# Kernel optimization log

Hardware: AMD Instinct MI355X
Metric: run time of the kernel (lower is better)

Reference implementation:

```python
import jax, jax.numpy as jnp
import numpy as np

D_MODEL = 2048
NHEAD = 32
GROUPS = 8
HEAD_DIM = D_MODEL // NHEAD  # 64
HPG = NHEAD // GROUPS        # heads per group = 4
ROPE_BASE = 10000.0


def _rope(x):
    # x: [B, H, S, D] -- rotate-half RoPE over full head dim, matching RoPE module
    S, D = x.shape[2], x.shape[3]
    theta = 1.0 / (ROPE_BASE ** (jnp.arange(0, D, 2, dtype=jnp.float32) / D))  # [D/2]
    idx_theta = jnp.arange(S, dtype=jnp.float32)[:, None] * theta[None, :]     # [S, D/2]
    ang = jnp.concatenate([idx_theta, idx_theta], axis=-1)                     # [S, D]
    cos = jnp.cos(ang)[None, None]  # [1,1,S,D]
    sin = jnp.sin(ang)[None, None]
    d2 = D // 2
    neg_half = jnp.concatenate([-x[..., d2:], x[..., :d2]], axis=-1)
    return x * cos + neg_half * sin


def setup_inputs() -> dict:
    key = jax.random.key(0)
    ks = jax.random.split(key, 9)
    B, S = 2, 2048
    s_in = 1.0 / np.sqrt(D_MODEL)
    return {
        "x": jax.random.normal(ks[0], (B, S, D_MODEL), jnp.float32),
        "Wq": jax.random.normal(ks[1], (D_MODEL, D_MODEL), jnp.float32) * s_in,
        "bq": jax.random.normal(ks[2], (D_MODEL,), jnp.float32) * 0.01,
        "Wk": jax.random.normal(ks[3], (HEAD_DIM * GROUPS, D_MODEL), jnp.float32) * s_in,
        "bk": jax.random.normal(ks[4], (HEAD_DIM * GROUPS,), jnp.float32) * 0.01,
        "Wv": jax.random.normal(ks[5], (HEAD_DIM * GROUPS, D_MODEL), jnp.float32) * s_in,
        "bv": jax.random.normal(ks[6], (HEAD_DIM * GROUPS,), jnp.float32) * 0.01,
        "Wo": jax.random.normal(ks[7], (D_MODEL, D_MODEL), jnp.float32) * s_in,
        "bo": jax.random.normal(ks[8], (D_MODEL,), jnp.float32) * 0.01,
    }


def reference(x, Wq, bq, Wk, bk, Wv, bv, Wo, bo):
    B, S, _ = x.shape
    # projections (torch Linear: x @ W.T + b)
    q = (x @ Wq.T + bq).reshape(B, S, NHEAD, HEAD_DIM).transpose(0, 2, 1, 3)   # [B,H,S,D]
    k = (x @ Wk.T + bk).reshape(B, S, GROUPS, HEAD_DIM).transpose(0, 2, 1, 3)  # [B,G,S,D]
    v = (x @ Wv.T + bv).reshape(B, S, GROUPS, HEAD_DIM).transpose(0, 2, 1, 3)  # [B,G,S,D]
    q = _rope(q)
    k = _rope(k)
    # grouped-query attention: share each k/v group across HPG query heads
    qg = q.reshape(B, GROUPS, HPG, S, HEAD_DIM)
    scale = 1.0 / np.sqrt(HEAD_DIM)
    scores = jnp.einsum('bghsd,bgtd->bghst', qg, k) * scale  # [B,G,Hpg,S,S]
    causal = jnp.tril(jnp.ones((S, S), dtype=bool))
    scores = jnp.where(causal, scores, jnp.finfo(scores.dtype).min)
    attn = jax.nn.softmax(scores, axis=-1)
    out = jnp.einsum('bghst,bgtd->bghsd', attn, v)           # [B,G,Hpg,S,D]
    out = out.reshape(B, NHEAD, S, HEAD_DIM).transpose(0, 2, 1, 3).reshape(B, S, D_MODEL)
    return out @ Wo.T + bo
```

## Files before the change

kernel.cpp:

```cpp
#include <hip/hip_runtime.h>

typedef unsigned short u16;
typedef __bf16 bf16x8 __attribute__((ext_vector_type(8)));
typedef float floatx4 __attribute__((ext_vector_type(4)));
typedef u16 u16x8 __attribute__((ext_vector_type(8)));
typedef u16 u16x4 __attribute__((ext_vector_type(4)));

#define D_MODEL 2048
#define S_LEN   2048
#define BATCH   2
#define NHEAD   32
#define GROUPS  8
#define HEAD_DIM 64
#define KV_DIM  512

__device__ __forceinline__ float bf2f(u16 h) {
  unsigned int u = ((unsigned int)h) << 16;
  return __builtin_bit_cast(float, u);
}
__device__ __forceinline__ u16 f2bf(float f) {
  unsigned int u = __builtin_bit_cast(unsigned int, f);
  u += 0x7fffu + ((u >> 16) & 1u);
  return (u16)(u >> 16);
}
__device__ __forceinline__ float fexp2(float x) {
  float r;
  asm("v_exp_f32 %0, %1" : "=v"(r) : "v"(x));
  return r;
}

#define GLD_LDS(gp, lp) \
  __builtin_amdgcn_global_load_lds((__attribute__((address_space(1))) void*)(gp), \
                                   (__attribute__((address_space(3))) void*)(lp), 16, 0, 0)

__global__ __launch_bounds__(256)
void cvt5_f32_bf16(const float* s0, const float* s1, const float* s2,
                   const float* s3, const float* s4,
                   u16* d0, u16* d1, u16* d2, u16* d3, u16* d4,
                   int n0, int n1, int n2, int n3, int n4,
                   float* ct, float* st)
{
  if (blockIdx.y == 5) {
    int idx = blockIdx.x * 256 + threadIdx.x;
    if (idx < S_LEN * 32) {
      int s = idx >> 5, d = idx & 31;
      float theta = __expf(-(float)d * 0.28782313662425574f);
      float sn, cs;
      sincosf((float)s * theta, &sn, &cs);
      ct[idx] = cs; st[idx] = sn;
    }
    return;
  }
  const float* s; u16* d; int n;
  switch (blockIdx.y) {
    case 0: s = s0; d = d0; n = n0; break;
    case 1: s = s1; d = d1; n = n1; break;
    case 2: s = s2; d = d2; n = n2; break;
    case 3: s = s3; d = d3; n = n3; break;
    default: s = s4; d = d4; n = n4; break;
  }
  long i = ((long)blockIdx.x * 256 + threadIdx.x) * 8;
  if (i >= n) return;
  floatx4 a = *(const floatx4*)(s + i);
  floatx4 b = *(const floatx4*)(s + i + 4);
  u16x8 r;
#pragma unroll
  for (int j = 0; j < 4; ++j) { r[j] = f2bf(a[j]); r[4 + j] = f2bf(b[j]); }
  *(u16x8*)(d + i) = r;
}

__global__ __launch_bounds__(256, 3)
void gemm_qkv(const u16* __restrict__ A, const u16* __restrict__ Wq,
              const u16* __restrict__ Wkv,
              const float* __restrict__ bq, const float* __restrict__ bk,
              const float* __restrict__ bv,
              u16* __restrict__ Qb, u16* __restrict__ Kb, u16* __restrict__ Vt,
              const float* __restrict__ ct, const float* __restrict__ st)
{
  const int K = D_MODEL;
  __shared__ __align__(16) u16 As[2 * 128 * 32];
  __shared__ __align__(16) u16 Bs[2 * 128 * 32];
  const int t = threadIdx.x;
  const int w = t >> 6, l = t & 63;
  const int lr = l & 15, lq = l >> 4;
  const int wm = (w >> 1) * 64, wn = (w & 1) * 64;
  const long bm = (long)blockIdx.x * 128;

  const bool isQ = blockIdx.y < 16;
  const long bn = isQ ? (long)blockIdx.y * 128 : (long)(blockIdx.y - 16) * 128;
  const u16* W = isQ ? Wq : Wkv;

  floatx4 acc[4][4] = {};

  const u16* a0 = A + (bm + (t >> 2)) * (long)K + (t & 3) * 8;
  const u16* a1 = a0 + 64L * K;
  const u16* pB0 = W + (bn + (t >> 2)) * (long)K + (t & 3) * 8;
  const u16* pB1 = pB0 + 64L * K;
  u16* As0 = As + w * 512;
  u16* As1 = As + 2048 + w * 512;
  u16* Bs0 = Bs + w * 512;
  u16* Bs1 = Bs + 2048 + w * 512;

  for (int k0 = 0; k0 < K; k0 += 64) {
    GLD_LDS(a0 + k0, As0);
    GLD_LDS(a1 + k0, As1);
    GLD_LDS(pB0 + k0, Bs0);
    GLD_LDS(pB1 + k0, Bs1);
    GLD_LDS(a0 + k0 + 32, As0 + 4096);
    GLD_LDS(a1 + k0 + 32, As1 + 4096);
    GLD_LDS(pB0 + k0 + 32, Bs0 + 4096);
    GLD_LDS(pB1 + k0 + 32, Bs1 + 4096);
    __syncthreads();

#pragma unroll
    for (int kk = 0; kk < 2; ++kk) {
      const u16* as = As + kk * 4096;
      const u16* bs = Bs + kk * 4096;
      bf16x8 av[4], bv8[4];
#pragma unroll
      for (int i = 0; i < 4; ++i)
        av[i] = *(const bf16x8*)(as + (wm + i * 16 + lr) * 32 + lq * 8);
#pragma unroll
      for (int j = 0; j < 4; ++j)
        bv8[j] = *(const bf16x8*)(bs + (wn + j * 16 + lr) * 32 + lq * 8);
#pragma unroll
      for (int i = 0; i < 4; ++i)
#pragma unroll
        for (int j = 0; j < 4; ++j)
          acc[i][j] = __builtin_amdgcn_mfma_f32_16x16x32_bf16(av[i], bv8[j], acc[i][j], 0, 0, 0);
    }
    __syncthreads();
  }

  if (isQ || bn < KV_DIM) {
    const float* bias = isQ ? bq : bk;
    u16* dst = isQ ? Qb : Kb;
    const long ldc = isQ ? D_MODEL : KV_DIM;
    float bb[4];
#pragma unroll
    for (int j = 0; j < 4; ++j)
      bb[j] = bias[bn + wn + j * 16 + lr];
#pragma unroll
    for (int i = 0; i < 4; ++i) {
#pragma unroll
      for (int rr = 0; rr < 4; ++rr) {
        long row = bm + wm + i * 16 + lq * 4 + rr;
        int srow = (int)row & (S_LEN - 1);
        float c0 = ct[srow * 32 + lr],      sn0 = st[srow * 32 + lr];
        float c1 = ct[srow * 32 + 16 + lr], sn1 = st[srow * 32 + 16 + lr];
        float v0 = acc[i][0][rr] + bb[0];
        float v1 = acc[i][1][rr] + bb[1];
        float v2 = acc[i][2][rr] + bb[2];
        float v3 = acc[i][3][rr] + bb[3];
        u16* cp = dst + row * ldc + bn + wn + lr;
        cp[0]  = f2bf(v0 * c0 - v2 * sn0);
        cp[16] = f2bf(v1 * c1 - v3 * sn1);
        cp[32] = f2bf(v2 * c0 + v0 * sn0);
        cp[48] = f2bf(v3 * c1 + v1 * sn1);
      }
    }
  } else {
    float bb[4];
#pragma unroll
    for (int j = 0; j < 4; ++j)
      bb[j] = bv[bn - KV_DIM + wn + j * 16 + lr];
#pragma unroll
    for (int i = 0; i < 4; ++i) {
      int row0 = (int)bm + wm + i * 16 + lq * 4;
      int b = row0 >> 11, s0r = row0 & (S_LEN - 1);
#pragma unroll
      for (int j = 0; j < 4; ++j) {
        int vcol = (int)bn - KV_DIM + wn + j * 16 + lr;
        u16x4 pv;
#pragma unroll
        for (int rr = 0; rr < 4; ++rr)
          pv[rr] = f2bf(acc[i][j][rr] + bb[j]);
        *(u16x4*)(Vt + ((long)b * KV_DIM + vcol) * S_LEN + s0r) = pv;
      }
    }
  }
}

__global__ __launch_bounds__(256, 3)
void gemm_out(const u16* __restrict__ A, const u16* __restrict__ W,
              const float* __restrict__ bias, float* __restrict__ C,
              int K, int ldc)
{
  __shared__ __align__(16) u16 As[2 * 128 * 32];
  __shared__ __align__(16) u16 Bs[2 * 128 * 32];
  const int t = threadIdx.x;
  const int w = t >> 6, l = t & 63;
  const int lr = l & 15, lq = l >> 4;
  const int wm = (w >> 1) * 64, wn = (w & 1) * 64;
  const long bm = (long)blockIdx.x * 128;
  const long bn = (long)blockIdx.y * 128;

  floatx4 acc[4][4] = {};

  const u16* a0 = A + (bm + (t >> 2)) * (long)K + (t & 3) * 8;
  const u16* a1 = a0 + 64L * K;
  const u16* pB0 = W + (bn + (t >> 2)) * (long)K + (t & 3) * 8;
  const u16* pB1 = pB0 + 64L * K;
  u16* As0 = As + w * 512;
  u16* As1 = As + 2048 + w * 512;
  u16* Bs0 = Bs + w * 512;
  u16* Bs1 = Bs + 2048 + w * 512;

  for (int k0 = 0; k0 < K; k0 += 64) {
    GLD_LDS(a0 + k0, As0);
    GLD_LDS(a1 + k0, As1);
    GLD_LDS(pB0 + k0, Bs0);
    GLD_LDS(pB1 + k0, Bs1);
    GLD_LDS(a0 + k0 + 32, As0 + 4096);
    GLD_LDS(a1 + k0 + 32, As1 + 4096);
    GLD_LDS(pB0 + k0 + 32, Bs0 + 4096);
    GLD_LDS(pB1 + k0 + 32, Bs1 + 4096);
    __syncthreads();

#pragma unroll
    for (int kk = 0; kk < 2; ++kk) {
      const u16* as = As + kk * 4096;
      const u16* bs = Bs + kk * 4096;
      bf16x8 av[4], bv[4];
#pragma unroll
      for (int i = 0; i < 4; ++i)
        av[i] = *(const bf16x8*)(as + (wm + i * 16 + lr) * 32 + lq * 8);
#pragma unroll
      for (int j = 0; j < 4; ++j)
        bv[j] = *(const bf16x8*)(bs + (wn + j * 16 + lr) * 32 + lq * 8);
#pragma unroll
      for (int i = 0; i < 4; ++i)
#pragma unroll
        for (int j = 0; j < 4; ++j)
          acc[i][j] = __builtin_amdgcn_mfma_f32_16x16x32_bf16(av[i], bv[j], acc[i][j], 0, 0, 0);
    }
    __syncthreads();
  }

  float bb[4];
#pragma unroll
  for (int j = 0; j < 4; ++j)
    bb[j] = bias[bn + wn + j * 16 + lr];
#pragma unroll
  for (int i = 0; i < 4; ++i) {
#pragma unroll
    for (int rr = 0; rr < 4; ++rr) {
      long row = bm + wm + i * 16 + lq * 4 + rr;
      long cidx = row * (long)ldc + bn + wn + lr;
      float* cp = C + cidx;
#pragma unroll
      for (int j = 0; j < 4; ++j)
        cp[j * 16] = acc[i][j][rr] + bb[j];
    }
  }
}

__global__ __launch_bounds__(256, 3)
void gqa_attn(const u16* Q, const u16* __restrict__ Kc,
              const u16* __restrict__ Vt, u16* O)
{
  __shared__ __align__(16) u16 KV[2][16 * 512];
  __shared__ __align__(16) u16 Ps[4][2][16 * 72];

  const int pr = blockIdx.x;
  const int bh = blockIdx.y;
  const int b = bh >> 5, h = bh & 31, g = h >> 2;

  const int t = threadIdx.x;
  const int w = t >> 6, l = t & 63;
  const int lr = l & 15, lq = l >> 4;

  const u16* Kp = Kc + ((long)b * S_LEN) * KV_DIM + g * HEAD_DIM;
  const u16* Vp = Vt + ((long)b * KV_DIM + g * HEAD_DIM) * S_LEN;

  long sb[4];
  {
    const int sig2 = ((l >> 2) ^ (l >> 4)) & 1;
    const int sig1 = ((l >> 1) ^ (l >> 3)) & 1;
    const int sig0 = (l ^ sig2) & 1;
    const int row = ((l >> 2) & 14) | sig2;
    const int cl = ((sig1 << 1) | sig0) * 8;
#pragma unroll
    for (int q = 0; q < 4; ++q) {
      const int r = (w & 1) * 4 + q;
      const int jj = r >> 1, cc = r & 1;
      sb[q] = (w < 2) ? ((long)(jj * 16 + row) * KV_DIM + cc * 32 + cl)
                      : ((long)(jj * 16 + row) * S_LEN + cc * 32 + cl);
    }
  }
  const u16* sp = (w < 2) ? Kp : Vp;
  const long smul = (w < 2) ? (long)64 * KV_DIM : 64;
  const int dbase = ((w < 2) ? 0 : 4096) + (w & 1) * 2048;
  const int koff = ((4 * lr + lq) ^ (lr & 7)) * 8;

  bf16x8 onesf;
#pragma unroll
  for (int e = 0; e < 8; ++e) onesf[e] = (__bf16)1.0f;

#define STAGE(bufi, kt_) do { \
    const long soff_ = (long)(kt_) * smul; \
    GLD_LDS(sp + soff_ + sb[0], &KV[bufi][dbase + 0 * 512]); \
    GLD_LDS(sp + soff_ + sb[1], &KV[bufi][dbase + 1 * 512]); \
    GLD_LDS(sp + soff_ + sb[2], &KV[bufi][dbase + 2 * 512]); \
    GLD_LDS(sp + soff_ + sb[3], &KV[bufi][dbase + 3 * 512]); \
  } while (0)

#define TILE(ktv, D0, D1) do { \
    const u16* buf_ = &KV[(ktv) & 1][0]; \
    floatx4 z0[4] = {}, z1[4] = {}; \
    _Pragma("unroll") \
    for (int j = 0; j < 4; ++j) { \
      bf16x8 kf0 = *(const bf16x8*)(buf_ + j * 1024 + koff); \
      bf16x8 kf1 = *(const bf16x8*)(buf_ + j * 1024 + 512 + koff); \
      if (!(D1) && (!(D0) || j <= w)) { \
        z0[j] = __builtin_amdgcn_mfma_f32_16x16x32_bf16(kf0, qf00, z0[j], 0, 0, 0); \
        z0[j] = __builtin_amdgcn_mfma_f32_16x16x32_bf16(kf1, qf01, z0[j], 0, 0, 0); \
      } \
      if (!(D1) || j <= w) { \
        z1[j] = __builtin_amdgcn_mfma_f32_16x16x32_bf16(kf0, qf10, z1[j], 0, 0, 0); \
        z1[j] = __builtin_amdgcn_mfma_f32_16x16x32_bf16(kf1, qf11, z1[j], 0, 0, 0); \
      } \
    } \
    if (!(D1)) { \
      _Pragma("unroll") \
      for (int j = 0; j < 4; ++j) { \
        u16x4 pk; \
        _Pragma("unroll") \
        for (int rr = 0; rr < 4; ++rr) { \
          float ps; \
          if ((D0) && (j * 16 + lq * 4 + rr > w * 16 + lr)) ps = 0.f; \
          else ps = fexp2(z0[j][rr] * 0.18033688011112042f - 23.083120654223414f); \
          pk[rr] = __builtin_bit_cast(u16, (__bf16)ps); \
        } \
        *(u16x4*)&Ps[w][0][lr * 72 + j * 16 + lq * 4] = pk; \
      } \
    } \
    _Pragma("unroll") \
    for (int j = 0; j < 4; ++j) { \
      u16x4 pk; \
      _Pragma("unroll") \
      for (int rr = 0; rr < 4; ++rr) { \
        float ps; \
        if ((D1) && (j * 16 + lq * 4 + rr > w * 16 + lr)) ps = 0.f; \
        else ps = fexp2(z1[j][rr] * 0.18033688011112042f - 23.083120654223414f); \
        pk[rr] = __builtin_bit_cast(u16, (__bf16)ps); \
      } \
      *(u16x4*)&Ps[w][1][lr * 72 + j * 16 + lq * 4] = pk; \
    } \
    bf16x8 pa00 = *(const bf16x8*)&Ps[w][0][lr * 72 + lq * 8]; \
    bf16x8 pa01 = *(const bf16x8*)&Ps[w][0][lr * 72 + 32 + lq * 8]; \
    bf16x8 pa10 = *(const bf16x8*)&Ps[w][1][lr * 72 + lq * 8]; \
    bf16x8 pa11 = *(const bf16x8*)&Ps[w][1][lr * 72 + 32 + lq * 8]; \
    if (!(D1)) { \
      lsa0 = __builtin_amdgcn_mfma_f32_16x16x32_bf16(pa00, onesf, lsa0, 0, 0, 0); \
      if (!(D0) || w >= 2) \
        lsa0 = __builtin_amdgcn_mfma_f32_16x16x32_bf16(pa01, onesf, lsa0, 0, 0, 0); \
    } \
    lsa1 = __builtin_amdgcn_mfma_f32_16x16x32_bf16(pa10, onesf, lsa1, 0, 0, 0); \
    if (!(D1) || w >= 2) \
      lsa1 = __builtin_amdgcn_mfma_f32_16x16x32_bf16(pa11, onesf, lsa1, 0, 0, 0); \
    const u16* vbuf_ = buf_ + 4096; \
    _Pragma("unroll") \
    for (int j = 0; j < 4; ++j) { \
      bf16x8 vb0 = *(const bf16x8*)(vbuf_ + j * 1024 + koff); \
      bf16x8 vb1 = *(const bf16x8*)(vbuf_ + j * 1024 + 512 + koff); \
      if (!(D1)) { \
        o0[j] = __builtin_amdgcn_mfma_f32_16x16x32_bf16(pa00, vb0, o0[j], 0, 0, 0); \
        if (!(D0) || w >= 2) \
          o0[j] = __builtin_amdgcn_mfma_f32_16x16x32_bf16(pa01, vb1, o0[j], 0, 0, 0); \
      } \
      o1[j] = __builtin_amdgcn_mfma_f32_16x16x32_bf16(pa10, vb0, o1[j], 0, 0, 0); \
      if (!(D1) || w >= 2) \
        o1[j] = __builtin_amdgcn_mfma_f32_16x16x32_bf16(pa11, vb1, o1[j], 0, 0, 0); \
    } \
  } while (0)

#pragma unroll 1
  for (int seg = 0; seg < 2; ++seg) {
    const int qt = seg ? (15 - pr) : pr;
    const u16* Qp = Q + ((long)b * S_LEN + qt * 128) * D_MODEL + h * HEAD_DIM;
    u16* Op = O + ((long)b * S_LEN + qt * 128) * D_MODEL + h * HEAD_DIM;

    bf16x8 qf00, qf01, qf10, qf11;
    {
      const u16* qr0 = Qp + (long)(w * 16 + lr) * D_MODEL;
      qf00 = *(const bf16x8*)(qr0 + lq * 8);
      qf01 = *(const bf16x8*)(qr0 + 32 + lq * 8);
      const u16* qr1 = qr0 + (long)64 * D_MODEL;
      qf10 = *(const bf16x8*)(qr1 + lq * 8);
      qf11 = *(const bf16x8*)(qr1 + 32 + lq * 8);
    }

    floatx4 o0[4] = {}, o1[4] = {};
    floatx4 lsa0 = {}, lsa1 = {};
    const int NKT = 2 * qt + 2;

    if (seg) __syncthreads();
    STAGE(0, 0);
    for (int kt = 0; kt < NKT - 2; ++kt) {
      __syncthreads();
      STAGE((kt + 1) & 1, kt + 1);
      TILE(kt, false, false);
    }
    __syncthreads();
    STAGE((NKT - 1) & 1, NKT - 1);
    TILE(NKT - 2, true, false);
    __syncthreads();
    TILE(NKT - 1, false, true);

#pragma unroll
    for (int s = 0; s < 2; ++s) {
      const floatx4 lsv = s ? lsa1 : lsa0;
      const floatx4* oo = s ? o1 : o0;
#pragma unroll
      for (int rr = 0; rr < 4; ++rr) {
        float inv = 1.f / lsv[rr];
        long row = s * 64 + w * 16 + lq * 4 + rr;
        u16* op = Op + row * (long)D_MODEL + lr;
#pragma unroll
        for (int j = 0; j < 4; ++j)
          op[j * 16] = f2bf(oo[j][rr] * inv);
      }
    }
  }
#undef TILE
#undef STAGE
}

extern "C" void kernel_launch(void* const* d_in, const int* in_sizes, int n_in,
                              void* d_out, int out_size, void* d_ws, size_t ws_size,
                              hipStream_t stream)
{
  const float* x  = (const float*)d_in[0];
  const float* Wq = (const float*)d_in[1];
  const float* bq = (const float*)d_in[2];
  const float* Wk = (const float*)d_in[3];
  const float* bk = (const float*)d_in[4];
  const float* Wv = (const float*)d_in[5];
  const float* bv = (const float*)d_in[6];
  const float* Wo = (const float*)d_in[7];
  const float* bo = (const float*)d_in[8];
  float* out = (float*)d_out;

  const int Sx  = BATCH * S_LEN * D_MODEL;
  const int SWq = D_MODEL * D_MODEL;
  const int SWk = KV_DIM * D_MODEL;
  const int SWv = KV_DIM * D_MODEL;
  const int SWo = D_MODEL * D_MODEL;

  u16* xb  = (u16*)d_ws;
  u16* Wqb = xb  + Sx;
  u16* Wkb = Wqb + SWq;
  u16* Wvb = Wkb + SWk;
  u16* Wob = Wvb + SWv;
  u16* Qb  = Wob + SWo;
  u16* Kb  = Qb + (size_t)4096 * 2048;
  u16* Vtb = Kb + (size_t)4096 * 512;
  float* ctab = (float*)(Vtb + (size_t)BATCH * KV_DIM * S_LEN);
  float* stab = ctab + S_LEN * 32;
  u16* AO  = Qb;

  const int M = BATCH * S_LEN;
  dim3 blk(256);
  cvt5_f32_bf16<<<dim3(4096, 6), blk, 0, stream>>>(x, Wq, Wk, Wv, Wo,
                                                   xb, Wqb, Wkb, Wvb, Wob,
                                                   Sx, SWq, SWk, SWv, SWo,
                                                   ctab, stab);
  gemm_qkv<<<dim3(M / 128, 24), blk, 0, stream>>>(xb, Wqb, Wkb, bq, bk, bv,
                                                  Qb, Kb, Vtb, ctab, stab);
  gqa_attn<<<dim3(8, BATCH * NHEAD), blk, 0, stream>>>(Qb, Kb, Vtb, AO);
  gemm_out<<<dim3(M / 128, D_MODEL / 128), blk, 0, stream>>>(AO, Wob, bo, out, D_MODEL, D_MODEL);
}
```

Before: 280.1 us.

## Process both paired query tiles concurrently with 512-thread attention blocks sharing K/V stages

The attention kernel previously processed two causal query tiles (pr and 15-pr) sequentially within a 256-thread block. It now launches 512 threads, with waves 0-3 handling the short tile and waves 4-7 the long tile, sharing each staged K/V tile so K/V is loaded once for both. Each wave stages half as much data. This removes the serial second pass and the duplicated K/V loads for the overlapping prefix. In exchange, the short-tile waves sit idle at barriers once their tile finishes, and launch bounds change to 512 threads with 4 waves per SIMD, which may tighten register limits.

Result: slower. 289.9 us (+3.5%).

```diff
diff --git a/kernel.cpp b/kernel.cpp
--- a/kernel.cpp
+++ b/kernel.cpp
@@ -255,12 +255,12 @@
   }
 }
 
-__global__ __launch_bounds__(256, 3)
+__global__ __launch_bounds__(512, 4)
 void gqa_attn(const u16* Q, const u16* __restrict__ Kc,
               const u16* __restrict__ Vt, u16* O)
 {
   __shared__ __align__(16) u16 KV[2][16 * 512];
-  __shared__ __align__(16) u16 Ps[4][2][16 * 72];
+  __shared__ __align__(16) u16 Ps[8][2][16 * 72];
 
   const int pr = blockIdx.x;
   const int bh = blockIdx.y;
@@ -268,12 +268,20 @@
 
   const int t = threadIdx.x;
   const int w = t >> 6, l = t & 63;
+  const int w4 = w & 3;
   const int lr = l & 15, lq = l >> 4;
+
+  const int qt = (w < 4) ? pr : (15 - pr);
+  const int NKTw = 2 * qt + 2;
+  const int NKTmax = 32 - 2 * pr;
 
   const u16* Kp = Kc + ((long)b * S_LEN) * KV_DIM + g * HEAD_DIM;
   const u16* Vp = Vt + ((long)b * KV_DIM + g * HEAD_DIM) * S_LEN;
-
-  long sb[4];
+  const u16* Qp = Q + ((long)b * S_LEN + qt * 128) * D_MODEL + h * HEAD_DIM;
+  u16* Op = O + ((long)b * S_LEN + qt * 128) * D_MODEL + h * HEAD_DIM;
+
+  const bool isK = (w < 4);
+  long sb[2];
   {
     const int sig2 = ((l >> 2) ^ (l >> 4)) & 1;
     const int sig1 = ((l >> 1) ^ (l >> 3)) & 1;
@@ -281,16 +289,14 @@
     const int row = ((l >> 2) & 14) | sig2;
     const int cl = ((sig1 << 1) | sig0) * 8;
 #pragma unroll
-    for (int q = 0; q < 4; ++q) {
-      const int r = (w & 1) * 4 + q;
-      const int jj = r >> 1, cc = r & 1;
-      sb[q] = (w < 2) ? ((long)(jj * 16 + row) * KV_DIM + cc * 32 + cl)
-                      : ((long)(jj * 16 + row) * S_LEN + cc * 32 + cl);
-    }
-  }
-  const u16* sp = (w < 2) ? Kp : Vp;
-  const long smul = (w < 2) ? (long)64 * KV_DIM : 64;
-  const int dbase = ((w < 2) ? 0 : 4096) + (w & 1) * 2048;
+    for (int q = 0; q < 2; ++q) {
+      sb[q] = isK ? ((long)(w4 * 16 + row) * KV_DIM + q * 32 + cl)
+                  : ((long)(w4 * 16 + row) * S_LEN + q * 32 + cl);
+    }
+  }
+  const u16* sp = isK ? Kp : Vp;
+  const long smul = isK ? (long)64 * KV_DIM : 64;
+  const int dbase = (isK ? 0 : 4096) + w4 * 1024;
   const int koff = ((4 * lr + lq) ^ (lr & 7)) * 8;
 
   bf16x8 onesf;
@@ -301,130 +307,117 @@
     const long soff_ = (long)(kt_) * smul; \
     GLD_LDS(sp + soff_ + sb[0], &KV[bufi][dbase + 0 * 512]); \
     GLD_LDS(sp + soff_ + sb[1], &KV[bufi][dbase + 1 * 512]); \
-    GLD_LDS(sp + soff_ + sb[2], &KV[bufi][dbase + 2 * 512]); \
-    GLD_LDS(sp + soff_ + sb[3], &KV[bufi][dbase + 3 * 512]); \
   } while (0)
 
-#define TILE(ktv, D0, D1) do { \
-    const u16* buf_ = &KV[(ktv) & 1][0]; \
-    floatx4 z0[4] = {}, z1[4] = {}; \
-    _Pragma("unroll") \
-    for (int j = 0; j < 4; ++j) { \
-      bf16x8 kf0 = *(const bf16x8*)(buf_ + j * 1024 + koff); \
-      bf16x8 kf1 = *(const bf16x8*)(buf_ + j * 1024 + 512 + koff); \
-      if (!(D1) && (!(D0) || j <= w)) { \
-        z0[j] = __builtin_amdgcn_mfma_f32_16x16x32_bf16(kf0, qf00, z0[j], 0, 0, 0); \
-        z0[j] = __builtin_amdgcn_mfma_f32_16x16x32_bf16(kf1, qf01, z0[j], 0, 0, 0); \
-      } \
-      if (!(D1) || j <= w) { \
-        z1[j] = __builtin_amdgcn_mfma_f32_16x16x32_bf16(kf0, qf10, z1[j], 0, 0, 0); \
-        z1[j] = __builtin_amdgcn_mfma_f32_16x16x32_bf16(kf1, qf11, z1[j], 0, 0, 0); \
-      } \
-    } \
-    if (!(D1)) { \
-      _Pragma("unroll") \
-      for (int j = 0; j < 4; ++j) { \
-        u16x4 pk; \
-        _Pragma("unroll") \
-        for (int rr = 0; rr < 4; ++rr) { \
-          float ps; \
-          if ((D0) && (j * 16 + lq * 4 + rr > w * 16 + lr)) ps = 0.f; \
-          else ps = fexp2(z0[j][rr] * 0.18033688011112042f - 23.083120654223414f); \
-          pk[rr] = __builtin_bit_cast(u16, (__bf16)ps); \
-        } \
-        *(u16x4*)&Ps[w][0][lr * 72 + j * 16 + lq * 4] = pk; \
-      } \
-    } \
-    _Pragma("unroll") \
-    for (int j = 0; j < 4; ++j) { \
-      u16x4 pk; \
-      _Pragma("unroll") \
-      for (int rr = 0; rr < 4; ++rr) { \
-        float ps; \
-        if ((D1) && (j * 16 + lq * 4 + rr > w * 16 + lr)) ps = 0.f; \
-        else ps = fexp2(z1[j][rr] * 0.18033688011112042f - 23.083120654223414f); \
-        pk[rr] = __builtin_bit_cast(u16, (__bf16)ps); \
-      } \
-      *(u16x4*)&Ps[w][1][lr * 72 + j * 16 + lq * 4] = pk; \
-    } \
-    bf16x8 pa00 = *(const bf16x8*)&Ps[w][0][lr * 72 + lq * 8]; \
-    bf16x8 pa01 = *(const bf16x8*)&Ps[w][0][lr * 72 + 32 + lq * 8]; \
-    bf16x8 pa10 = *(const bf16x8*)&Ps[w][1][lr * 72 + lq * 8]; \
-    bf16x8 pa11 = *(const bf16x8*)&Ps[w][1][lr * 72 + 32 + lq * 8]; \
-    if (!(D1)) { \
-      lsa0 = __builtin_amdgcn_mfma_f32_16x16x32_bf16(pa00, onesf, lsa0, 0, 0, 0); \
-      if (!(D0) || w >= 2) \
-        lsa0 = __builtin_amdgcn_mfma_f32_16x16x32_bf16(pa01, onesf, lsa0, 0, 0, 0); \
-    } \
-    lsa1 = __builtin_amdgcn_mfma_f32_16x16x32_bf16(pa10, onesf, lsa1, 0, 0, 0); \
-    if (!(D1) || w >= 2) \
-      lsa1 = __builtin_amdgcn_mfma_f32_16x16x32_bf16(pa11, onesf, lsa1, 0, 0, 0); \
-    const u16* vbuf_ = buf_ + 4096; \
-    _Pragma("unroll") \
-    for (int j = 0; j < 4; ++j) { \
-      bf16x8 vb0 = *(const bf16x8*)(vbuf_ + j * 1024 + koff); \
-      bf16x8 vb1 = *(const bf16x8*)(vbuf_ + j * 1024 + 512 + koff); \
-      if (!(D1)) { \
-        o0[j] = __builtin_amdgcn_mfma_f32_16x16x32_bf16(pa00, vb0, o0[j], 0, 0, 0); \
-        if (!(D0) || w >= 2) \
-          o0[j] = __builtin_amdgcn_mfma_f32_16x16x32_bf16(pa01, vb1, o0[j], 0, 0, 0); \
-      } \
-      o1[j] = __builtin_amdgcn_mfma_f32_16x16x32_bf16(pa10, vb0, o1[j], 0, 0, 0); \
-      if (!(D1) || w >= 2) \
-        o1[j] = __builtin_amdgcn_mfma_f32_16x16x32_bf16(pa11, vb1, o1[j], 0, 0, 0); \
-    } \
-  } while (0)
-
+  bf16x8 qf00, qf01, qf10, qf11;
+  {
+    const u16* qr0 = Qp + (long)(w4 * 16 + lr) * D_MODEL;
+    qf00 = *(const bf16x8*)(qr0 + lq * 8);
+    qf01 = *(const bf16x8*)(qr0 + 32 + lq * 8);
+    const u16* qr1 = qr0 + (long)64 * D_MODEL;
+    qf10 = *(const bf16x8*)(qr1 + lq * 8);
+    qf11 = *(const bf16x8*)(qr1 + 32 + lq * 8);
+  }
+
+  floatx4 o0[4] = {}, o1[4] = {};
+  floatx4 lsa0 = {}, lsa1 = {};
+
+  STAGE(0, 0);
 #pragma unroll 1
-  for (int seg = 0; seg < 2; ++seg) {
-    const int qt = seg ? (15 - pr) : pr;
-    const u16* Qp = Q + ((long)b * S_LEN + qt * 128) * D_MODEL + h * HEAD_DIM;
-    u16* Op = O + ((long)b * S_LEN + qt * 128) * D_MODEL + h * HEAD_DIM;
-
-    bf16x8 qf00, qf01, qf10, qf11;
-    {
-      const u16* qr0 = Qp + (long)(w * 16 + lr) * D_MODEL;
-      qf00 = *(const bf16x8*)(qr0 + lq * 8);
-      qf01 = *(const bf16x8*)(qr0 + 32 + lq * 8);
-      const u16* qr1 = qr0 + (long)64 * D_MODEL;
-      qf10 = *(const bf16x8*)(qr1 + lq * 8);
-      qf11 = *(const bf16x8*)(qr1 + 32 + lq * 8);
-    }
-
-    floatx4 o0[4] = {}, o1[4] = {};
-    floatx4 lsa0 = {}, lsa1 = {};
-    const int NKT = 2 * qt + 2;
-
-    if (seg) __syncthreads();
-    STAGE(0, 0);
-    for (int kt = 0; kt < NKT - 2; ++kt) {
-      __syncthreads();
-      STAGE((kt + 1) & 1, kt + 1);
-      TILE(kt, false, false);
-    }
+  for (int kt = 0; kt < NKTmax; ++kt) {
     __syncthreads();
-    STAGE((NKT - 1) & 1, NKT - 1);
-    TILE(NKT - 2, true, false);
-    __syncthreads();
-    TILE(NKT - 1, false, true);
-
-#pragma unroll
-    for (int s = 0; s < 2; ++s) {
-      const floatx4 lsv = s ? lsa1 : lsa0;
-      const floatx4* oo = s ? o1 : o0;
+    if (kt + 1 < NKTmax) STAGE((kt + 1) & 1, kt + 1);
+    if (kt >= NKTw) continue;
+
+    const bool D0 = (kt == NKTw - 2);
+    const bool D1 = (kt == NKTw - 1);
+    const u16* buf_ = &KV[kt & 1][0];
+
+    floatx4 z0[4] = {}, z1[4] = {};
+#pragma unroll
+    for (int j = 0; j < 4; ++j) {
+      bf16x8 kf0 = *(const bf16x8*)(buf_ + j * 1024 + koff);
+      bf16x8 kf1 = *(const bf16x8*)(buf_ + j * 1024 + 512 + koff);
+      if (!D1 && (!D0 || j <= w4)) {
+        z0[j] = __builtin_amdgcn_mfma_f32_16x16x32_bf16(kf0, qf00, z0[j], 0, 0, 0);
+        z0[j] = __builtin_amdgcn_mfma_f32_16x16x32_bf16(kf1, qf01, z0[j], 0, 0, 0);
+      }
+      if (!D1 || j <= w4) {
+        z1[j] = __builtin_amdgcn_mfma_f32_16x16x32_bf16(kf0, qf10, z1[j], 0, 0, 0);
+        z1[j] = __builtin_amdgcn_mfma_f32_16x16x32_bf16(kf1, qf11, z1[j], 0, 0, 0);
+      }
+    }
+
+    if (!D1) {
+#pragma unroll
+      for (int j = 0; j < 4; ++j) {
+        u16x4 pk;
+#pragma unroll
+        for (int rr = 0; rr < 4; ++rr) {
+          float ps = fexp2(z0[j][rr] * 0.18033688011112042f - 23.083120654223414f);
+          if (D0 && (j * 16 + lq * 4 + rr > w4 * 16 + lr)) ps = 0.f;
+          pk[rr] = __builtin_bit_cast(u16, (__bf16)ps);
+        }
+        *(u16x4*)&Ps[w][0][lr * 72 + j * 16 + lq * 4] = pk;
+      }
+    }
+#pragma unroll
+    for (int j = 0; j < 4; ++j) {
+      u16x4 pk;
 #pragma unroll
       for (int rr = 0; rr < 4; ++rr) {
-        float inv = 1.f / lsv[rr];
-        long row = s * 64 + w * 16 + lq * 4 + rr;
-        u16* op = Op + row * (long)D_MODEL + lr;
-#pragma unroll
-        for (int j = 0; j < 4; ++j)
-          op[j * 16] = f2bf(oo[j][rr] * inv);
-      }
-    }
-  }
-#undef TILE
+        float ps = fexp2(z1[j][rr] * 0.18033688011112042f - 23.083120654223414f);
+        if (D1 && (j * 16 + lq * 4 + rr > w4 * 16 + lr)) ps = 0.f;
+        pk[rr] = __builtin_bit_cast(u16, (__bf16)ps);
+      }
+      *(u16x4*)&Ps[w][1][lr * 72 + j * 16 + lq * 4] = pk;
+    }
+
+    bf16x8 pa00 = *(const bf16x8*)&Ps[w][0][lr * 72 + lq * 8];
+    bf16x8 pa01 = *(const bf16x8*)&Ps[w][0][lr * 72 + 32 + lq * 8];
+    bf16x8 pa10 = *(const bf16x8*)&Ps[w][1][lr * 72 + lq * 8];
+    bf16x8 pa11 = *(const bf16x8*)&Ps[w][1][lr * 72 + 32 + lq * 8];
+
+    if (!D1) {
+      lsa0 = __builtin_amdgcn_mfma_f32_16x16x32_bf16(pa00, onesf, lsa0, 0, 0, 0);
+      if (!D0 || w4 >= 2)
+        lsa0 = __builtin_amdgcn_mfma_f32_16x16x32_bf16(pa01, onesf, lsa0, 0, 0, 0);
+    }
+    lsa1 = __builtin_amdgcn_mfma_f32_16x16x32_bf16(pa10, onesf, lsa1, 0, 0, 0);
+    if (!D1 || w4 >= 2)
+      lsa1 = __builtin_amdgcn_mfma_f32_16x16x32_bf16(pa11, onesf, lsa1, 0, 0, 0);
+
+    const u16* vbuf_ = buf_ + 4096;
+#pragma unroll
+    for (int j = 0; j < 4; ++j) {
+      bf16x8 vb0 = *(const bf16x8*)(vbuf_ + j * 1024 + koff);
+      bf16x8 vb1 = *(const bf16x8*)(vbuf_ + j * 1024 + 512 + koff);
+      if (!D1) {
+        o0[j] = __builtin_amdgcn_mfma_f32_16x16x32_bf16(pa00, vb0, o0[j], 0, 0, 0);
+        if (!D0 || w4 >= 2)
+          o0[j] = __builtin_amdgcn_mfma_f32_16x16x32_bf16(pa01, vb1, o0[j], 0, 0, 0);
+      }
+      o1[j] = __builtin_amdgcn_mfma_f32_16x16x32_bf16(pa10, vb0, o1[j], 0, 0, 0);
+      if (!D1 || w4 >= 2)
+        o1[j] = __builtin_amdgcn_mfma_f32_16x16x32_bf16(pa11, vb1, o1[j], 0, 0, 0);
+    }
+  }
 #undef STAGE
+
+#pragma unroll
+  for (int s = 0; s < 2; ++s) {
+    const floatx4 lsv = s ? lsa1 : lsa0;
+    const floatx4* oo = s ? o1 : o0;
+#pragma unroll
+    for (int rr = 0; rr < 4; ++rr) {
+      float inv = 1.f / lsv[rr];
+      long row = s * 64 + w4 * 16 + lq * 4 + rr;
+      u16* op = Op + row * (long)D_MODEL + lr;
+#pragma unroll
+      for (int j = 0; j < 4; ++j)
+        op[j * 16] = f2bf(oo[j][rr] * inv);
+    }
+  }
 }
 
 extern "C" void kernel_launch(void* const* d_in, const int* in_sizes, int n_in,
@@ -468,6 +461,6 @@
                                                    ctab, stab);
   gemm_qkv<<<dim3(M / 128, 24), blk, 0, stream>>>(xb, Wqb, Wkb, bq, bk, bv,
                                                   Qb, Kb, Vtb, ctab, stab);
-  gqa_attn<<<dim3(8, BATCH * NHEAD), blk, 0, stream>>>(Qb, Kb, Vtb, AO);
+  gqa_attn<<<dim3(8, BATCH * NHEAD), dim3(512), 0, stream>>>(Qb, Kb, Vtb, AO);
   gemm_out<<<dim3(M / 128, D_MODEL / 128), blk, 0, stream>>>(AO, Wob, bo, out, D_MODEL, D_MODEL);
 }
```
